# Performance work log

Hardware: AMD Instinct MI355X
Metric: run time of the kernel (lower is better)

## Reference

```python
import jax, jax.numpy as jnp
import numpy as np

B, C3, H3, W3 = 8, 512, 24, 24
C5, H5, W5 = 256, 96, 96
GRIDS = (6, 3, 2, 1)
GROUPS = 2


def conv2d(x, w):
    # stride-1 'same' conv (matches torch autopad k//2 for odd k), NCHW/OIHW
    return jax.lax.conv_general_dilated(x, w, (1, 1), 'SAME',
                                        dimension_numbers=('NCHW', 'OIHW', 'NCHW'))


def conv_bn_silu(x, w):
    # ultralytics-style Conv = Conv2d(bias=False) + BatchNorm2d + SiLU.
    # BN in eval with default running stats (mean=0, var=1, gamma=1, beta=0) is identity.
    return jax.nn.silu(conv2d(x, w))


def psp(x):
    # adaptive_avg_pool2d to (g, g) for each grid; H,W divisible by all grids -> equal bins
    b, c, h, w = x.shape
    outs = []
    for g in GRIDS:
        outs.append(x.reshape(b, c, g, h // g, g, w // g).mean(axis=(3, 5)).reshape(b, c, g * g))
    return jnp.concatenate(outs, axis=2)  # [b, c, 36+9+4+1=50]


def resize_bilinear_ac(x, oh, ow):
    # F.interpolate(mode='bilinear', align_corners=True)
    n, c, h, w = x.shape
    ys = jnp.linspace(0.0, h - 1.0, oh)
    xs = jnp.linspace(0.0, w - 1.0, ow)
    y0 = jnp.clip(jnp.floor(ys).astype(jnp.int32), 0, h - 2)
    x0 = jnp.clip(jnp.floor(xs).astype(jnp.int32), 0, w - 2)
    wy = (ys - y0)[None, None, :, None]
    wx = (xs - x0)[None, None, None, :]
    xr = jnp.take(x, y0, axis=2) * (1 - wy) + jnp.take(x, y0 + 1, axis=2) * wy
    return jnp.take(xr, x0, axis=3) * (1 - wx) + jnp.take(xr, x0 + 1, axis=3) * wx


def grid_sample(img, grid):
    # F.grid_sample bilinear, align_corners=True, padding_mode='zeros'
    # img [N,C,H,W], grid [N,Ho,Wo,2] with (x,y) normalized coords
    n, c, h, w = img.shape
    gx = (grid[..., 0] + 1.0) * 0.5 * (w - 1)
    gy = (grid[..., 1] + 1.0) * 0.5 * (h - 1)
    x0 = jnp.floor(gx)
    y0 = jnp.floor(gy)
    wx1 = gx - x0
    wy1 = gy - y0
    flat = img.reshape(n, c, h * w)

    def gather(xi, yi, wgt):
        valid = (xi >= 0) & (xi <= w - 1) & (yi >= 0) & (yi <= h - 1)
        xc = jnp.clip(xi, 0, w - 1).astype(jnp.int32)
        yc = jnp.clip(yi, 0, h - 1).astype(jnp.int32)
        idx = (yc * w + xc).reshape(n, 1, -1)
        v = jnp.take_along_axis(flat, idx, axis=2).reshape(n, c, grid.shape[1], grid.shape[2])
        return v * (wgt * valid)[:, None]

    return (gather(x0, y0, (1 - wx1) * (1 - wy1)) + gather(x0 + 1, y0, wx1 * (1 - wy1))
            + gather(x0, y0 + 1, (1 - wx1) * wy1) + gather(x0 + 1, y0 + 1, wx1 * wy1))


def _w(key, shape):
    fan_in = int(np.prod(shape[1:]))
    return (jax.random.normal(key, shape, jnp.float32) / np.sqrt(fan_in)).astype(jnp.float32)


def setup_inputs() -> dict:
    key = jax.random.key(0)
    ks = jax.random.split(key, 17)
    return {
        'p3': jax.random.normal(ks[0], (B, C3, H3, W3), jnp.float32),
        'p5': jax.random.normal(ks[1], (B, C5, H5, W5), jnp.float32),
        # CFC_CRB
        'w_red': _w(ks[2], (C3, C3, 3, 3)),
        'wq': _w(ks[3], (32, C3, 1, 1)), 'bq': jnp.zeros((32,), jnp.float32),
        'wk': _w(ks[4], (32, C3)), 'bk': jnp.zeros((32,), jnp.float32),
        'wv': _w(ks[5], (C3, C3)), 'bv': jnp.zeros((C3,), jnp.float32),
        'la_w1': _w(ks[6], (C3 // 8, C3, 1, 1)),
        'la_w2': _w(ks[7], (C3, C3 // 8, 3, 3)),
        # SFC_G2
        'w32': _w(ks[8], (C5, C3, 3, 3)),
        'w8': _w(ks[9], (C5, C5, 3, 3)),
        'woff1': _w(ks[10], (64, 2 * C5, 1, 1)),
        'woff2': _w(ks[11], (GROUPS * 4 + 2, 64, 3, 3)),
    }


def reference(p3, p5, w_red, wq, bq, wk, bk, wv, bv, la_w1, la_w2, w32, w8, woff1, woff2):
    # ---------------- CFC_CRB ----------------
    x = conv_bn_silu(p3, w_red)                      # [b,512,h,w]
    b, c, h, w = x.shape
    q = conv2d(x, wq) + bq[None, :, None, None]       # [b,32,h,w]
    q = q.reshape(b, 32, h * w).transpose(0, 2, 1)    # [b,N,32]
    kfeat = psp(x)                                    # [b,512,50]
    k = jnp.einsum('oc,bcm->bom', wk, kfeat) + bk[None, :, None]   # [b,32,50]
    sim = jax.nn.softmax(jnp.einsum('bnc,bcm->bnm', q, k), axis=-1)  # [b,N,50]
    v = jnp.einsum('oc,bcm->bom', wv, kfeat) + bv[None, :, None]   # [b,512,50]
    context = jnp.einsum('bcm,bnm->bcn', v, sim).reshape(b, c, h, w)
    # LocalAttenModule: res1 * tanh(conv(context)) + res2
    mask = jnp.tanh(conv2d(conv_bn_silu(context, la_w1), la_w2))
    context = context * mask + context
    p3o = x + context                                 # [b,512,24,24]

    # ---------------- SFC_G2 ----------------
    sp = conv_bn_silu(p3o, w32)                       # [b,256,24,24]
    sp = resize_bilinear_ac(sp, H5, W5)               # [b,256,96,96]
    cp = conv_bn_silu(p5, w8)                         # [b,256,96,96]
    cr = conv2d(conv_bn_silu(jnp.concatenate([cp, sp], axis=1), woff1), woff2)  # [b,10,96,96]

    n = b
    spg = sp.reshape(n * GROUPS, -1, H5, W5)
    cpg = cp.reshape(n * GROUPS, -1, H5, W5)
    off_l = cr[:, 0:GROUPS * 2].reshape(n * GROUPS, 2, H5, W5)
    off_h = cr[:, GROUPS * 2:GROUPS * 4].reshape(n * GROUPS, 2, H5, W5)

    gx = jnp.linspace(-1.0, 1.0, W5)
    gy = jnp.linspace(-1.0, 1.0, H5)
    X, Y = jnp.meshgrid(gx, gy)                       # [H5,W5] each
    base = jnp.stack([X, Y], axis=-1)[None]           # [1,H5,W5,2] (x,y)
    norm = jnp.array([W5, H5], dtype=sp.dtype)
    grid_l = base + off_l.transpose(0, 2, 3, 1) / norm
    grid_h = base + off_h.transpose(0, 2, 3, 1) / norm

    cps = grid_sample(cpg, grid_l).reshape(n, -1, H5, W5)
    sps = grid_sample(spg, grid_h).reshape(n, -1, H5, W5)
    att = 1.0 + jnp.tanh(cr[:, GROUPS * 4:])          # [b,2,H,W]
    p5o = sps * att[:, 0:1] + cps * att[:, 1:2]
    return (p3o, p5o)
```

## Files before the change

### kernel.cpp

```cpp
#include <hip/hip_runtime.h>
#include <math.h>

#define DI __device__ __forceinline__

typedef __attribute__((ext_vector_type(8))) short bf16x8;
typedef __attribute__((ext_vector_type(4))) float f32x4;

DI float silu_f(float v) { return v / (1.f + __expf(-v)); }
DI float4 ld4(const float* p) { return *reinterpret_cast<const float4*>(p); }
DI void st4(float* p, const float4& v) { *reinterpret_cast<float4*>(p) = v; }
DI unsigned short f2bf(float f) {
    unsigned u = __float_as_uint(f);
    unsigned r = (u + 0x7FFFu + ((u >> 16) & 1u)) >> 16;
    return (unsigned short)r;
}
DI float bf2f(unsigned short u) { return __uint_as_float(((unsigned)u) << 16); }

__global__ void pack_w2_kernel(const float* __restrict__ w, unsigned short* __restrict__ pk,
                               int Ci, int Co, int COG) {
    int idx = blockIdx.x * 256 + threadIdx.x;
    int total = Ci * Co * 9;
    if (idx >= total) return;
    int cc = idx & 31;
    int t = idx >> 5;
    int col = t % COG; t /= COG;
    int dydx = t % 9;  t /= 9;
    int nCoG = Co / COG;
    int cog = t % nCoG;
    int ch = t / nCoG;
    int co = cog * COG + col;
    pk[idx] = f2bf(w[((size_t)co * Ci + (ch << 5) + cc) * 9 + dydx]);
}

__global__ void pack_w1_kernel(const float* __restrict__ w, unsigned short* __restrict__ pk) {
    int idx = blockIdx.x * 256 + threadIdx.x;
    if (idx >= 32768) return;
    int cc = idx & 31;
    int col = (idx >> 5) & 63;
    int ch = idx >> 11;
    pk[idx] = f2bf(w[(size_t)col * 512 + (ch << 5) + cc]);
}

__global__ void pack_in_kernel(const float* __restrict__ in, unsigned short* __restrict__ pk,
                               int Ci, int HW, int total) {
    int idx = blockIdx.x * 256 + threadIdx.x;
    if (idx >= total) return;
    const int nCh = Ci >> 5;
    int cg = idx & 3;
    int t = idx >> 2;
    int pix = t % HW; t /= HW;
    int ch = t % nCh;
    int b = t / nCh;
    const float* src = in + ((size_t)b * Ci + (ch << 5) + (cg << 3)) * HW + pix;
    unsigned p[4];
#pragma unroll
    for (int j = 0; j < 4; ++j) {
        float v0 = src[(size_t)(2 * j) * HW];
        float v1 = src[(size_t)(2 * j + 1) * HW];
        p[j] = (unsigned)f2bf(v0) | ((unsigned)f2bf(v1) << 16);
    }
    *(uint4*)&pk[(((size_t)b * nCh + ch) * HW + pix) * 32 + (cg << 3)] =
        make_uint4(p[0], p[1], p[2], p[3]);
}

template <int TH, int TW, int BF, int WCO, int FUSE, int OUTPK>
__global__ void __launch_bounds__(256)
conv3x3_mfma2(const unsigned short* __restrict__ pin, const unsigned short* __restrict__ wpk,
              float* __restrict__ out, unsigned short* __restrict__ outpk,
              int B, int Ci, int Co, int H, int W,
              const float* __restrict__ ctx, const float* __restrict__ xres) {
    static_assert(TH * TW == 4 * BF * 16, "tile px = 4 waves * BF frags * 16");
    constexpr int COG = WCO * 16;
    constexpr int TWH = TW + 2;
    constexpr int HP = (TH + 2) * TWH;
    __shared__ __align__(16) unsigned short lin[HP * 40];

    const int nTx = W / TW, nTy = H / TH, nCoG = Co / COG;
    const int nwg = gridDim.x;
    int wg = (blockIdx.x & 7) * (nwg >> 3) + (blockIdx.x >> 3);
    const int cog = wg % nCoG; wg /= nCoG;
    const int tx = wg % nTx;   wg /= nTx;
    const int ty = wg % nTy;
    const int b = wg / nTy;
    const int ox = tx * TW, oy = ty * TH, co0 = cog * COG;

    const int tid = threadIdx.x;
    const int wave = tid >> 6, lane = tid & 63;
    const int l15 = lane & 15, g = lane >> 4;
    const int wpx = wave * (BF * 16);

    int rr[BF], cc_[BF];
#pragma unroll
    for (int bf = 0; bf < BF; ++bf) {
        int px = wpx + bf * 16 + l15;
        rr[bf] = px / TW;
        cc_[bf] = px % TW;
    }

    f32x4 acc[WCO][BF];
#pragma unroll
    for (int af = 0; af < WCO; ++af)
#pragma unroll
        for (int bf = 0; bf < BF; ++bf) acc[af][bf] = {};

    const int nCh = Ci >> 5;
    const size_t HWs = (size_t)H * W;

    for (int ch = 0; ch < nCh; ++ch) {
#pragma unroll
        for (int it = 0; it < (HP * 4 + 255) / 256; ++it) {
            int e = tid + it * 256;
            if (e < HP * 4) {
                int cg = e & 3;
                int hp = e >> 2;
                int hy = hp / TWH, hx = hp % TWH;
                int gy = oy + hy - 1, gx = ox + hx - 1;
                uint4 v = make_uint4(0, 0, 0, 0);
                if ((unsigned)gy < (unsigned)H && (unsigned)gx < (unsigned)W)
                    v = *(const uint4*)&pin[(((size_t)b * nCh + ch) * H * W
                                            + (size_t)gy * W + gx) * 32 + (cg << 3)];
                *(uint4*)&lin[hp * 40 + (cg << 3)] = v;
            }
        }
        __syncthreads();

        const unsigned short* wbase =
            wpk + ((((size_t)ch * nCoG + cog) * 9) * COG + l15) * 32 + g * 8;
#pragma unroll
        for (int dy = 0; dy < 3; ++dy) {
#pragma unroll
            for (int dx = 0; dx < 3; ++dx) {
                const int dydx = dy * 3 + dx;
                bf16x8 a[WCO];
#pragma unroll
                for (int af = 0; af < WCO; ++af)
                    a[af] = *(const bf16x8*)(wbase + ((size_t)dydx * COG + af * 16) * 32);
                bf16x8 bb[BF];
#pragma unroll
                for (int bf = 0; bf < BF; ++bf)
                    bb[bf] = *(const bf16x8*)&lin[((rr[bf] + dy) * TWH + cc_[bf] + dx) * 40 + g * 8];
#pragma unroll
                for (int af = 0; af < WCO; ++af)
#pragma unroll
                    for (int bf = 0; bf < BF; ++bf)
                        acc[af][bf] = __builtin_amdgcn_mfma_f32_16x16x32_bf16(
                            a[af], bb[bf], acc[af][bf], 0, 0, 0);
            }
        }
        __syncthreads();
    }
    const int nChO = Co >> 5;
#pragma unroll
    for (int af = 0; af < WCO; ++af) {
#pragma unroll
        for (int bf = 0; bf < BF; ++bf) {
            int px = wpx + bf * 16 + l15;
            int y = oy + px / TW, x = ox + px % TW;
            size_t pixg = (size_t)y * W + x;
            int coB = co0 + af * 16 + (g << 2);
            float vv[4];
#pragma unroll
            for (int r4 = 0; r4 < 4; ++r4) {
                float v = acc[af][bf][r4];
                if (FUSE == 1) v = silu_f(v);
                else if (FUSE == 2) {
                    size_t base = ((size_t)b * Co + coB + r4) * HWs + pixg;
                    v = xres[base] + ctx[base] * (1.f + tanhf(v));
                }
                vv[r4] = v;
            }
            if (OUTPK != 1) {
#pragma unroll
                for (int r4 = 0; r4 < 4; ++r4)
                    out[((size_t)b * Co + coB + r4) * HWs + pixg] = vv[r4];
            }
            if (OUTPK >= 1) {
                ushort4 s;
                s.x = f2bf(vv[0]); s.y = f2bf(vv[1]); s.z = f2bf(vv[2]); s.w = f2bf(vv[3]);
                *(ushort4*)&outpk[(((size_t)b * nChO + (coB >> 5)) * HWs + pixg) * 32 + (coB & 31)] = s;
            }
        }
    }
}

__global__ void __launch_bounds__(256)
cat_mfma(const unsigned short* __restrict__ cp_pk, const unsigned short* __restrict__ sp_pk,
         const unsigned short* __restrict__ wpk, float* __restrict__ out) {
    __shared__ __align__(16) unsigned short lin1[128 * 36];
    const int nwg = gridDim.x;
    int wg = (blockIdx.x & 7) * (nwg >> 3) + (blockIdx.x >> 3);
    int mt = wg % 72;
    int b = wg / 72;
    int m0 = mt * 128;
    const int tid = threadIdx.x;
    const int wave = tid >> 6, lane = tid & 63;
    const int l15 = lane & 15, g = lane >> 4;
    const int wpx = wave * 32;

    f32x4 acc[4][2];
#pragma unroll
    for (int af = 0; af < 4; ++af)
#pragma unroll
        for (int bf = 0; bf < 2; ++bf) acc[af][bf] = {};

    for (int ch = 0; ch < 16; ++ch) {
        const unsigned short* src = (ch < 8)
            ? cp_pk + (((size_t)b * 8 + ch) * 9216 + m0) * 32
            : sp_pk + (((size_t)b * 8 + ch - 8) * 9216 + m0) * 32;
#pragma unroll
        for (int it = 0; it < 2; ++it) {
            int e = tid + it * 256;
            int px = e >> 2, cg = e & 3;
            *(uint4*)&lin1[px * 36 + (cg << 3)] = *(const uint4*)&src[px * 32 + (cg << 3)];
        }
        __syncthreads();
        const unsigned short* wb = wpk + ((size_t)ch * 64 + l15) * 32 + g * 8;
        bf16x8 a[4];
#pragma unroll
        for (int af = 0; af < 4; ++af)
            a[af] = *(const bf16x8*)(wb + (af * 16) * 32);
        bf16x8 bb[2];
#pragma unroll
        for (int bf = 0; bf < 2; ++bf)
            bb[bf] = *(const bf16x8*)&lin1[(wpx + bf * 16 + l15) * 36 + g * 8];
#pragma unroll
        for (int af = 0; af < 4; ++af)
#pragma unroll
            for (int bf = 0; bf < 2; ++bf)
                acc[af][bf] = __builtin_amdgcn_mfma_f32_16x16x32_bf16(
                    a[af], bb[bf], acc[af][bf], 0, 0, 0);
        __syncthreads();
    }
#pragma unroll
    for (int af = 0; af < 4; ++af) {
#pragma unroll
        for (int bf = 0; bf < 2; ++bf) {
            int m = m0 + wpx + bf * 16 + l15;
#pragma unroll
            for (int r4 = 0; r4 < 4; ++r4) {
                int o = af * 16 + (g << 2) + r4;
                out[((size_t)b * 64 + o) * 9216 + m] = silu_f(acc[af][bf][r4]);
            }
        }
    }
}

DI void gs_params(int x, int y, float ox, float oy, float4* w, int2* p) {
    const float S = 47.5f / 96.f;
    float px = x + ox * S;
    float py = y + oy * S;
    float fx0 = floorf(px), fy0 = floorf(py);
    float wx = px - fx0, wy = py - fy0;
    float vx0 = (fx0 >= 0.f && fx0 <= 95.f) ? 1.f : 0.f;
    float vx1 = (fx0 >= -1.f && fx0 <= 94.f) ? 1.f : 0.f;
    float vy0 = (fy0 >= 0.f && fy0 <= 95.f) ? 1.f : 0.f;
    float vy1 = (fy0 >= -1.f && fy0 <= 94.f) ? 1.f : 0.f;
    int x0 = (int)fminf(fmaxf(fx0, 0.f), 95.f);
    int x1 = (int)fminf(fmaxf(fx0 + 1.f, 0.f), 95.f);
    int y0 = (int)fminf(fmaxf(fy0, 0.f), 95.f);
    int y1 = (int)fminf(fmaxf(fy0 + 1.f, 0.f), 95.f);
    w->x = (1.f - wx) * (1.f - wy) * vx0 * vy0;
    w->y = wx * (1.f - wy) * vx1 * vy0;
    w->z = (1.f - wx) * wy * vx0 * vy1;
    w->w = wx * wy * vx1 * vy1;
    *p = make_int2(x0 | (x1 << 16), y0 | (y1 << 16));
}

template <int TH, int TW, int CO_BLK, int CO_T, int CIC, int FUSE>
__global__ void __launch_bounds__(576)
conv3x3_kernel(const float* __restrict__ in, const float* __restrict__ wgt,
               float* __restrict__ out, int B, int Ci, int Co, int H, int W,
               float4* __restrict__ wpar, int2* __restrict__ ipk,
               float2* __restrict__ attp) {
    constexpr int TWH = TW + 2;
    constexpr int TWP = TW + 3;
    constexpr int SPAT = TH * (TW / 4);
    __shared__ float lin[CIC][TH + 2][TWP];
    __shared__ float wls[CIC][9][CO_BLK];
    __shared__ float crs[10][TH * TW + 1];

    const int nTx = W / TW, nTy = H / TH;
    const int nCoG = (Co + CO_BLK - 1) / CO_BLK;
    int bid = blockIdx.x;
    const int cog = bid % nCoG; bid /= nCoG;
    const int tx = bid % nTx;   bid /= nTx;
    const int ty = bid % nTy;
    const int b = bid / nTy;
    const int ox = tx * TW, oy = ty * TH;
    const int co0 = cog * CO_BLK;

    const int tid = threadIdx.x;
    const int cot = tid / SPAT;
    const int sp = tid % SPAT;
    const int r = sp / (TW / 4);
    const int cg = sp % (TW / 4);

    float acc[4][4];
#pragma unroll
    for (int i = 0; i < 4; ++i)
#pragma unroll
        for (int j = 0; j < 4; ++j) acc[i][j] = 0.f;

    for (int ci0 = 0; ci0 < Ci; ci0 += CIC) {
        for (int e = tid; e < CIC * (TH + 2) * TWH; e += SPAT * CO_T) {
            int xx = e % TWH;
            int yy = (e / TWH) % (TH + 2);
            int cc = e / (TWH * (TH + 2));
            int gy = oy - 1 + yy, gx = ox - 1 + xx;
            float v = 0.f;
            if (gy >= 0 && gy < H && gx >= 0 && gx < W)
                v = in[(((size_t)b * Ci + ci0 + cc) * H + gy) * W + gx];
            lin[cc][yy][xx] = v;
        }
        for (int e = tid; e < CIC * 9 * CO_BLK; e += SPAT * CO_T) {
            int col = e % CO_BLK;
            int k = (e / CO_BLK) % 9;
            int cc = e / (CO_BLK * 9);
            int co = co0 + col;
            float v = 0.f;
            if (co < Co) v = wgt[((size_t)co * Ci + ci0 + cc) * 9 + k];
            wls[cc][k][col] = v;
        }
        __syncthreads();
#pragma unroll
        for (int cc = 0; cc < CIC; ++cc) {
            float v0[3][6];
#pragma unroll
            for (int ky = 0; ky < 3; ++ky)
#pragma unroll
                for (int u = 0; u < 6; ++u)
                    v0[ky][u] = lin[cc][r + ky][cg * 4 + u];
#pragma unroll
            for (int ky = 0; ky < 3; ++ky)
#pragma unroll
                for (int kx = 0; kx < 3; ++kx) {
                    const float4 w4 = ld4(&wls[cc][ky * 3 + kx][cot * 4]);
                    const float wv_[4] = {w4.x, w4.y, w4.z, w4.w};
#pragma unroll
                    for (int i = 0; i < 4; ++i)
#pragma unroll
                        for (int j = 0; j < 4; ++j)
                            acc[i][j] = fmaf(wv_[i], v0[ky][kx + j], acc[i][j]);
                }
        }
        __syncthreads();
    }
    if (FUSE == 3) {
#pragma unroll
        for (int i = 0; i < 4; ++i) {
            int co = co0 + cot * 4 + i;
            if (co >= 10) continue;
#pragma unroll
            for (int j = 0; j < 4; ++j)
                crs[co][r * TW + cg * 4 + j] = acc[i][j];
        }
        __syncthreads();
        for (int e = tid; e < TH * TW; e += SPAT * CO_T) {
            int xx = ox + (e % TW), yy = oy + (e / TW);
            int pixg = yy * 96 + xx;
            float4 w; int2 p;
#pragma unroll
            for (int g2 = 0; g2 < 2; ++g2) {
                gs_params(xx, yy, crs[2 * g2][e], crs[2 * g2 + 1][e], &w, &p);
                size_t el = ((size_t)g2 * 8 + b) * 9216 + pixg;
                wpar[el] = w; ipk[el] = p;
                gs_params(xx, yy, crs[4 + 2 * g2][e], crs[5 + 2 * g2][e], &w, &p);
                size_t eh = ((size_t)(2 + g2) * 8 + b) * 9216 + pixg;
                wpar[eh] = w; ipk[eh] = p;
            }
            float2 at;
            at.x = 1.f + tanhf(crs[8][e]);
            at.y = 1.f + tanhf(crs[9][e]);
            attp[(size_t)b * 9216 + pixg] = at;
        }
    } else {
        const int y = oy + r;
        const int xb = ox + cg * 4;
#pragma unroll
        for (int i = 0; i < 4; ++i) {
            int co = co0 + cot * 4 + i;
            if (co >= Co) continue;
            size_t base = (((size_t)b * Co + co) * H + y) * W + xb;
            float4 res;
            res.x = acc[i][0]; res.y = acc[i][1]; res.z = acc[i][2]; res.w = acc[i][3];
            st4(&out[base], res);
        }
    }
}

template <int ACT, int PK>
__global__ void __launch_bounds__(256)
gemm_om(const float* __restrict__ W, const float* __restrict__ bias,
        const float* __restrict__ in, float* __restrict__ out,
        unsigned short* __restrict__ pko,
        int B, int C, int O, int M, int nOt, int nMt) {
    __shared__ float xs[32][66];
    __shared__ float wls[64][33];
    int bid = blockIdx.x;
    int mt = bid % nMt; bid /= nMt;
    int ot = bid % nOt;
    int b  = bid / nOt;
    int o0 = ot * 64, m0 = mt * 64;
    int tid = threadIdx.x;
    int m_t = tid & 15, o_g = tid >> 4;
    float acc[4][4];
#pragma unroll
    for (int i = 0; i < 4; ++i)
#pragma unroll
        for (int j = 0; j < 4; ++j) acc[i][j] = 0.f;

    for (int c0 = 0; c0 < C; c0 += 32) {
#pragma unroll
        for (int it = 0; it < 8; ++it) {
            int e = tid + it * 256;
            int mm = e & 63, cc = e >> 6;
            float v = 0.f;
            if (m0 + mm < M) v = in[((size_t)b * C + c0 + cc) * M + m0 + mm];
            xs[cc][mm] = v;
        }
#pragma unroll
        for (int it = 0; it < 8; ++it) {
            int e = tid + it * 256;
            int cc = e & 31, ol = e >> 5;
            float v = 0.f;
            if (o0 + ol < O) v = W[(size_t)(o0 + ol) * C + c0 + cc];
            wls[ol][cc] = v;
        }
        __syncthreads();
#pragma unroll
        for (int cc = 0; cc < 32; ++cc) {
            float xv[4], wv[4];
#pragma unroll
            for (int j = 0; j < 4; ++j) xv[j] = xs[cc][j * 16 + m_t];
#pragma unroll
            for (int i = 0; i < 4; ++i) wv[i] = wls[o_g * 4 + i][cc];
#pragma unroll
            for (int i = 0; i < 4; ++i)
#pragma unroll
                for (int j = 0; j < 4; ++j)
                    acc[i][j] = fmaf(wv[i], xv[j], acc[i][j]);
        }
        __syncthreads();
    }
#pragma unroll
    for (int i = 0; i < 4; ++i) {
        int o = o0 + o_g * 4 + i;
        if (o >= O) continue;
        float bv = bias ? bias[o] : 0.f;
#pragma unroll
        for (int j = 0; j < 4; ++j) {
            int m = m0 + j * 16 + m_t;
            if (m >= M) continue;
            float v = acc[i][j] + bv;
            if (ACT == 1) v = silu_f(v);
            if (PK)
                pko[(((size_t)b * (O >> 5) + (o >> 5)) * M + m) * 32 + (o & 31)] = f2bf(v);
            else
                out[((size_t)b * O + o) * M + m] = v;
        }
    }
}

__global__ void psp_kernel(const float* __restrict__ x, float* __restrict__ kf) {
    __shared__ float pl[576];
    int bc = blockIdx.x;
    const float* xp = x + (size_t)bc * 576;
    for (int e = threadIdx.x; e < 576; e += 64) pl[e] = xp[e];
    __syncthreads();
    int m = threadIdx.x;
    if (m < 50) {
        int g, i0;
        if (m < 36)      { g = 6; i0 = m; }
        else if (m < 45) { g = 3; i0 = m - 36; }
        else if (m < 49) { g = 2; i0 = m - 45; }
        else             { g = 1; i0 = 0; }
        int bs = 24 / g;
        int by = i0 / g, bx = i0 % g;
        float s = 0.f;
        for (int yy = 0; yy < bs; ++yy)
            for (int xx = 0; xx < bs; ++xx)
                s += pl[(by * bs + yy) * 24 + bx * bs + xx];
        kf[(size_t)bc * 50 + m] = s / (float)(bs * bs);
    }
}

__global__ void __launch_bounds__(256)
sim_kernel(const float* __restrict__ q, const float* __restrict__ k,
           float* __restrict__ simg) {
    __shared__ float qs[32][65];
    __shared__ float ks[32][52];
    __shared__ float sm[64][52];
    int b = blockIdx.x / 9, n0 = (blockIdx.x % 9) * 64;
    int tid = threadIdx.x;
    for (int e = tid; e < 32 * 64; e += 256) {
        int c = e >> 6, n = e & 63;
        qs[c][n] = q[((size_t)b * 32 + c) * 576 + n0 + n];
    }
    for (int e = tid; e < 32 * 50; e += 256) {
        int c = e / 50, m = e % 50;
        ks[c][m] = k[((size_t)b * 32 + c) * 50 + m];
    }
    __syncthreads();
    for (int e = tid; e < 64 * 50; e += 256) {
        int n = e / 50, m = e % 50;
        float s = 0.f;
#pragma unroll
        for (int c = 0; c < 32; ++c) s = fmaf(qs[c][n], ks[c][m], s);
        sm[n][m] = s;
    }
    __syncthreads();
    if (tid < 64) {
        float mx = -1e30f;
        for (int m = 0; m < 50; ++m) mx = fmaxf(mx, sm[tid][m]);
        float sum = 0.f;
        for (int m = 0; m < 50; ++m) {
            float e2 = __expf(sm[tid][m] - mx);
            sm[tid][m] = e2;
            sum += e2;
        }
        float inv = 1.f / sum;
        for (int m = 0; m < 50; ++m) sm[tid][m] *= inv;
    }
    __syncthreads();
    for (int e = tid; e < 64 * 50; e += 256) {
        int n = e / 50, m = e % 50;
        simg[((size_t)b * 576 + n0 + n) * 50 + m] = sm[n][m];
    }
}

__global__ void __launch_bounds__(256)
ctx_kernel(const float* __restrict__ v, const float* __restrict__ simg,
           float* __restrict__ ctx) {
    __shared__ float vs[128][54];
    __shared__ float ss[64][54];
    int blk = blockIdx.x;
    int ct = blk & 3; blk >>= 2;
    int nt = blk % 9;
    int b = blk / 9;
    int c0 = ct * 128, n0 = nt * 64;
    int tid = threadIdx.x;
    for (int e = tid; e < 128 * 50; e += 256) {
        int c = e / 50, m = e % 50;
        vs[c][m] = v[((size_t)b * 512 + c0 + c) * 50 + m];
    }
    for (int e = tid; e < 64 * 50; e += 256) {
        int n = e / 50, m = e % 50;
        ss[n][m] = simg[((size_t)b * 576 + n0 + n) * 50 + m];
    }
    __syncthreads();
    int n_t = tid & 15;
    int c_t = tid >> 4;
    float acc[8][4];
#pragma unroll
    for (int i = 0; i < 8; ++i)
#pragma unroll
        for (int j = 0; j < 4; ++j) acc[i][j] = 0.f;
    for (int m = 0; m < 50; ++m) {
        float sv[4];
#pragma unroll
        for (int j = 0; j < 4; ++j) sv[j] = ss[j * 16 + n_t][m];
#pragma unroll
        for (int i = 0; i < 8; ++i) {
            float vv = vs[c_t * 8 + i][m];
#pragma unroll
            for (int j = 0; j < 4; ++j) acc[i][j] = fmaf(vv, sv[j], acc[i][j]);
        }
    }
#pragma unroll
    for (int i = 0; i < 8; ++i)
#pragma unroll
        for (int j = 0; j < 4; ++j)
            ctx[((size_t)b * 512 + c0 + c_t * 8 + i) * 576 + n0 + j * 16 + n_t] = acc[i][j];
}

__global__ void upsample2_kernel(const float* __restrict__ in, unsigned short* __restrict__ outpk) {
    int idx = blockIdx.x * 256 + threadIdx.x;
    if (idx >= 8 * 8 * 4 * 9216) return;
    int cg = idx & 3;
    int t = idx >> 2;
    int pix = t % 9216; t /= 9216;
    int ch = t & 7;
    int b = t >> 3;
    int x = pix % 96, y = pix / 96;
    float fy = y * (23.f / 95.f);
    float fx = x * (23.f / 95.f);
    int y0 = (int)fy; if (y0 > 22) y0 = 22;
    int x0 = (int)fx; if (x0 > 22) x0 = 22;
    float wy = fy - y0, wx = fx - x0;
    const float* base = in + ((size_t)b * 256 + ch * 32 + cg * 8) * 576 + y0 * 24 + x0;
    unsigned short s[8];
#pragma unroll
    for (int j = 0; j < 8; ++j) {
        const float* ip = base + (size_t)j * 576;
        float a = ip[0], bb = ip[1], c = ip[24], d = ip[25];
        float l = a * (1.f - wy) + c * wy;
        float r = bb * (1.f - wy) + d * wy;
        s[j] = f2bf(l * (1.f - wx) + r * wx);
    }
    *(uint4*)&outpk[(((size_t)b * 8 + ch) * 9216 + pix) * 32 + cg * 8] =
        make_uint4((unsigned)s[0] | ((unsigned)s[1] << 16),
                   (unsigned)s[2] | ((unsigned)s[3] << 16),
                   (unsigned)s[4] | ((unsigned)s[5] << 16),
                   (unsigned)s[6] | ((unsigned)s[7] << 16));
}

__global__ void __launch_bounds__(256)
gsample3_kernel(const unsigned short* __restrict__ cp_pk, const unsigned short* __restrict__ sp_pk,
                const float4* __restrict__ wpar, const int2* __restrict__ ipk,
                const float2* __restrict__ attp, float* __restrict__ p5o) {
    int idx = blockIdx.x * 256 + threadIdx.x;
    if (idx >= 8 * 32 * 9216) return;
    int pix = idx % 9216;
    int cb = (idx / 9216) & 31;
    int b = idx / (9216 * 32);
    int c0 = cb * 8;
    int g = c0 >> 7, ch = c0 >> 5, coff = c0 & 31;
    size_t el = ((size_t)g * 8 + b) * 9216 + pix;
    size_t eh = ((size_t)(2 + g) * 8 + b) * 9216 + pix;
    float4 wl = wpar[el]; int2 pl = ipk[el];
    float4 wh = wpar[eh]; int2 ph = ipk[eh];
    float2 at = attp[(size_t)b * 9216 + pix];
    int l00 = (pl.y & 0xffff) * 96 + (pl.x & 0xffff);
    int l01 = (pl.y & 0xffff) * 96 + (pl.x >> 16);
    int l10 = (pl.y >> 16) * 96 + (pl.x & 0xffff);
    int l11 = (pl.y >> 16) * 96 + (pl.x >> 16);
    int h00 = (ph.y & 0xffff) * 96 + (ph.x & 0xffff);
    int h01 = (ph.y & 0xffff) * 96 + (ph.x >> 16);
    int h10 = (ph.y >> 16) * 96 + (ph.x & 0xffff);
    int h11 = (ph.y >> 16) * 96 + (ph.x >> 16);
    const unsigned short* cb0 = cp_pk + (((size_t)b * 8 + ch) * 9216) * 32 + coff;
    const unsigned short* sb0 = sp_pk + (((size_t)b * 8 + ch) * 9216) * 32 + coff;
    ushort4 tc0 = *(const ushort4*)&cb0[(size_t)l00 * 32];
    ushort4 tc0b = *(const ushort4*)&cb0[(size_t)l00 * 32 + 4];
    ushort4 tc1 = *(const ushort4*)&cb0[(size_t)l01 * 32];
    ushort4 tc1b = *(const ushort4*)&cb0[(size_t)l01 * 32 + 4];
    ushort4 tc2 = *(const ushort4*)&cb0[(size_t)l10 * 32];
    ushort4 tc2b = *(const ushort4*)&cb0[(size_t)l10 * 32 + 4];
    ushort4 tc3 = *(const ushort4*)&cb0[(size_t)l11 * 32];
    ushort4 tc3b = *(const ushort4*)&cb0[(size_t)l11 * 32 + 4];
    ushort4 ts0 = *(const ushort4*)&sb0[(size_t)h00 * 32];
    ushort4 ts0b = *(const ushort4*)&sb0[(size_t)h00 * 32 + 4];
    ushort4 ts1 = *(const ushort4*)&sb0[(size_t)h01 * 32];
    ushort4 ts1b = *(const ushort4*)&sb0[(size_t)h01 * 32 + 4];
    ushort4 ts2 = *(const ushort4*)&sb0[(size_t)h10 * 32];
    ushort4 ts2b = *(const ushort4*)&sb0[(size_t)h10 * 32 + 4];
    ushort4 ts3 = *(const ushort4*)&sb0[(size_t)h11 * 32];
    ushort4 ts3b = *(const ushort4*)&sb0[(size_t)h11 * 32 + 4];
    const unsigned short* c0a = (const unsigned short*)&tc0;
    const unsigned short* c0bp = (const unsigned short*)&tc0b;
    const unsigned short* c1a = (const unsigned short*)&tc1;
    const unsigned short* c1bp = (const unsigned short*)&tc1b;
    const unsigned short* c2a = (const unsigned short*)&tc2;
    const unsigned short* c2bp = (const unsigned short*)&tc2b;
    const unsigned short* c3a = (const unsigned short*)&tc3;
    const unsigned short* c3bp = (const unsigned short*)&tc3b;
    const unsigned short* s0a = (const unsigned short*)&ts0;
    const unsigned short* s0bp = (const unsigned short*)&ts0b;
    const unsigned short* s1a = (const unsigned short*)&ts1;
    const unsigned short* s1bp = (const unsigned short*)&ts1b;
    const unsigned short* s2a = (const unsigned short*)&ts2;
    const unsigned short* s2bp = (const unsigned short*)&ts2b;
    const unsigned short* s3a = (const unsigned short*)&ts3;
    const unsigned short* s3bp = (const unsigned short*)&ts3b;
    float* op = p5o + ((size_t)b * 256 + c0) * 9216 + pix;
#pragma unroll
    for (int i = 0; i < 8; ++i) {
        unsigned short v0 = (i < 4) ? c0a[i] : c0bp[i - 4];
        unsigned short v1 = (i < 4) ? c1a[i] : c1bp[i - 4];
        unsigned short v2 = (i < 4) ? c2a[i] : c2bp[i - 4];
        unsigned short v3 = (i < 4) ? c3a[i] : c3bp[i - 4];
        float cps = wl.x * bf2f(v0) + wl.y * bf2f(v1) + wl.z * bf2f(v2) + wl.w * bf2f(v3);
        unsigned short u0 = (i < 4) ? s0a[i] : s0bp[i - 4];
        unsigned short u1 = (i < 4) ? s1a[i] : s1bp[i - 4];
        unsigned short u2 = (i < 4) ? s2a[i] : s2bp[i - 4];
        unsigned short u3 = (i < 4) ? s3a[i] : s3bp[i - 4];
        float sps = wh.x * bf2f(u0) + wh.y * bf2f(u1) + wh.z * bf2f(u2) + wh.w * bf2f(u3);
        op[(size_t)i * 9216] = sps * at.x + cps * at.y;
    }
}

extern "C" void kernel_launch(void* const* d_in, const int* in_sizes, int n_in,
                              void* d_out, int out_size, void* d_ws, size_t ws_size,
                              hipStream_t stream) {
    const float* p3    = (const float*)d_in[0];
    const float* p5    = (const float*)d_in[1];
    const float* w_red = (const float*)d_in[2];
    const float* wq    = (const float*)d_in[3];
    const float* bq    = (const float*)d_in[4];
    const float* wk    = (const float*)d_in[5];
    const float* bk    = (const float*)d_in[6];
    const float* wv    = (const float*)d_in[7];
    const float* bv    = (const float*)d_in[8];
    const float* la_w1 = (const float*)d_in[9];
    const float* la_w2 = (const float*)d_in[10];
    const float* w32   = (const float*)d_in[11];
    const float* w8    = (const float*)d_in[12];
    const float* woff1 = (const float*)d_in[13];
    const float* woff2 = (const float*)d_in[14];

    float* out = (float*)d_out;
    float* p3o = out;
    float* p5o = out + 2359296;

    float* ws = (float*)d_ws;
    float* x_   = ws + 0;
    float* ctx  = ws + 2359296;
    float* q    = ws + 4718592;
    float* kf   = ws + 4866048;
    float* km   = ws + 5070848;
    float* vm   = ws + 5083648;
    unsigned short* la1_pk = (unsigned short*)(ws + 5288448);
    float* sp24 = ws + 5435904;
    float4* wpar = (float4*)(ws + 6615552);
    int2*   ipk  = (int2*)(ws + 7795200);
    float2* attp = (float2*)(ws + 8385024);
    unsigned short* sp96_pk = (unsigned short*)(ws + 8601600);
    unsigned short* cp_pk   = (unsigned short*)(ws + 18038784);
    unsigned short* p5_pk   = (unsigned short*)(ws + 27475968);
    unsigned short* p3_pk   = (unsigned short*)(ws + 36913152);
    unsigned short* wred_pk = (unsigned short*)(ws + 38092800);
    unsigned short* w32_pk  = (unsigned short*)(ws + 39272448);
    unsigned short* w8_pk   = (unsigned short*)(ws + 39862272);
    unsigned short* wla2_pk = (unsigned short*)(ws + 40157184);
    unsigned short* woff1_pk= (unsigned short*)(ws + 40304640);
    float* simg = ws + 5288448 + 160000;
    simg = ws + 40321024;
    float* t64  = ws + 0;

    pack_w2_kernel<<<dim3(2359296 / 256), dim3(256), 0, stream>>>(w_red, wred_pk, 512, 512, 32);
    pack_w2_kernel<<<dim3(1179648 / 256), dim3(256), 0, stream>>>(w32, w32_pk, 512, 256, 16);
    pack_w2_kernel<<<dim3(589824 / 256), dim3(256), 0, stream>>>(w8, w8_pk, 256, 256, 64);
    pack_w2_kernel<<<dim3(294912 / 256), dim3(256), 0, stream>>>(la_w2, wla2_pk, 64, 512, 32);
    pack_w1_kernel<<<dim3(128), dim3(256), 0, stream>>>(woff1, woff1_pk);
    pack_in_kernel<<<dim3(2359296 / 256), dim3(256), 0, stream>>>(p5, p5_pk, 256, 9216, 2359296);
    pack_in_kernel<<<dim3(294912 / 256), dim3(256), 0, stream>>>(p3, p3_pk, 512, 576, 294912);

    conv3x3_mfma2<16, 16, 4, 4, 1, 1><<<dim3(1152), dim3(256), 0, stream>>>(
        p5_pk, w8_pk, nullptr, cp_pk, 8, 256, 256, 96, 96, nullptr, nullptr);
    conv3x3_mfma2<8, 24, 3, 2, 1, 0><<<dim3(384), dim3(256), 0, stream>>>(
        p3_pk, wred_pk, x_, nullptr, 8, 512, 512, 24, 24, nullptr, nullptr);
    gemm_om<0, 0><<<dim3(72), dim3(256), 0, stream>>>(
        wq, bq, x_, q, nullptr, 8, 512, 32, 576, 1, 9);
    psp_kernel<<<dim3(8 * 512), dim3(64), 0, stream>>>(x_, kf);
    gemm_om<0, 0><<<dim3(8), dim3(256), 0, stream>>>(
        wk, bk, kf, km, nullptr, 8, 512, 32, 50, 1, 1);
    gemm_om<0, 0><<<dim3(64), dim3(256), 0, stream>>>(
        wv, bv, kf, vm, nullptr, 8, 512, 512, 50, 8, 1);
    sim_kernel<<<dim3(72), dim3(256), 0, stream>>>(q, km, simg);
    ctx_kernel<<<dim3(288), dim3(256), 0, stream>>>(vm, simg, ctx);
    gemm_om<1, 1><<<dim3(72), dim3(256), 0, stream>>>(
        la_w1, nullptr, ctx, nullptr, la1_pk, 8, 512, 64, 576, 1, 9);
    conv3x3_mfma2<8, 24, 3, 2, 2, 2><<<dim3(384), dim3(256), 0, stream>>>(
        la1_pk, wla2_pk, p3o, p3_pk, 8, 64, 512, 24, 24, ctx, x_);
    conv3x3_mfma2<8, 24, 3, 1, 1, 0><<<dim3(384), dim3(256), 0, stream>>>(
        p3_pk, w32_pk, sp24, nullptr, 8, 512, 256, 24, 24, nullptr, nullptr);
    upsample2_kernel<<<dim3(9216), dim3(256), 0, stream>>>(sp24, sp96_pk);
    cat_mfma<<<dim3(576), dim3(256), 0, stream>>>(cp_pk, sp96_pk, woff1_pk, t64);
    conv3x3_kernel<8, 32, 12, 3, 4, 3><<<dim3(288), dim3(192), 0, stream>>>(
        t64, woff2, nullptr, 8, 64, 10, 96, 96, wpar, ipk, attp);
    gsample3_kernel<<<dim3(9216), dim3(256), 0, stream>>>(
        cp_pk, sp96_pk, wpar, ipk, attp, p5o);
}
```

Baseline: 893.2 us.

## Double-buffer conv3x3 LDS staging with direct global-to-LDS loads on padded inputs

Packed bf16 conv inputs are now stored with a one-pixel zero border, so the 3x3 conv tiles can be staged without bounds checks. Staging uses global_load_lds straight into two ping-pong LDS buffers with an XOR swizzle, which lets the load of the next channel chunk overlap the MFMA work on the current one and halves the barriers. The cost is extra memsets of the padded buffers on every call, a larger workspace layout, and doubled LDS use that may lower occupancy.

```diff
diff --git a/kernel.cpp b/kernel.cpp
--- a/kernel.cpp
+++ b/kernel.cpp
@@ -15,6 +15,12 @@
     return (unsigned short)r;
 }
 DI float bf2f(unsigned short u) { return __uint_as_float(((unsigned)u) << 16); }
+
+DI void gload_lds16(const unsigned short* g, unsigned short* l) {
+    __builtin_amdgcn_global_load_lds(
+        (const __attribute__((address_space(1))) void*)g,
+        (__attribute__((address_space(3))) void*)l, 16, 0, 0);
+}
 
 __global__ void pack_w2_kernel(const float* __restrict__ w, unsigned short* __restrict__ pk,
                                int Ci, int Co, int COG) {
@@ -41,16 +47,18 @@
     pk[idx] = f2bf(w[(size_t)col * 512 + (ch << 5) + cc]);
 }
 
-__global__ void pack_in_kernel(const float* __restrict__ in, unsigned short* __restrict__ pk,
-                               int Ci, int HW, int total) {
+__global__ void pack_in_pad_kernel(const float* __restrict__ in, unsigned short* __restrict__ pk,
+                                   int Ci, int H, int W, int total) {
     int idx = blockIdx.x * 256 + threadIdx.x;
     if (idx >= total) return;
     const int nCh = Ci >> 5;
+    const int HW = H * W;
     int cg = idx & 3;
     int t = idx >> 2;
     int pix = t % HW; t /= HW;
     int ch = t % nCh;
     int b = t / nCh;
+    int y = pix / W, x = pix % W;
     const float* src = in + ((size_t)b * Ci + (ch << 5) + (cg << 3)) * HW + pix;
     unsigned p[4];
 #pragma unroll
@@ -59,13 +67,13 @@
         float v1 = src[(size_t)(2 * j + 1) * HW];
         p[j] = (unsigned)f2bf(v0) | ((unsigned)f2bf(v1) << 16);
     }
-    *(uint4*)&pk[(((size_t)b * nCh + ch) * HW + pix) * 32 + (cg << 3)] =
-        make_uint4(p[0], p[1], p[2], p[3]);
-}
-
-template <int TH, int TW, int BF, int WCO, int FUSE, int OUTPK>
+    size_t dst = (((size_t)b * nCh + ch) * (H + 2) + (y + 1)) * (W + 2) + (x + 1);
+    *(uint4*)&pk[dst * 32 + (cg << 3)] = make_uint4(p[0], p[1], p[2], p[3]);
+}
+
+template <int TH, int TW, int BF, int WCO, int FUSE, int OUTPK, int OUTPAD>
 __global__ void __launch_bounds__(256)
-conv3x3_mfma2(const unsigned short* __restrict__ pin, const unsigned short* __restrict__ wpk,
+conv3x3_mfma3(const unsigned short* __restrict__ pin, const unsigned short* __restrict__ wpk,
               float* __restrict__ out, unsigned short* __restrict__ outpk,
               int B, int Ci, int Co, int H, int W,
               const float* __restrict__ ctx, const float* __restrict__ xres) {
@@ -73,9 +81,14 @@
     constexpr int COG = WCO * 16;
     constexpr int TWH = TW + 2;
     constexpr int HP = (TH + 2) * TWH;
-    __shared__ __align__(16) unsigned short lin[HP * 40];
+    constexpr int NG = HP * 4;
+    constexpr int NIT = (NG + 255) / 256;
+    static_assert(NG % 8 == 0, "granules divisible by 8");
+    __shared__ __align__(16) unsigned short linA[NG * 8];
+    __shared__ __align__(16) unsigned short linB[NG * 8];
 
     const int nTx = W / TW, nTy = H / TH, nCoG = Co / COG;
+    const int Wp = W + 2, Hp = H + 2;
     const int nwg = gridDim.x;
     int wg = (blockIdx.x & 7) * (nwg >> 3) + (blockIdx.x >> 3);
     const int cog = wg % nCoG; wg /= nCoG;
@@ -85,9 +98,9 @@
     const int ox = tx * TW, oy = ty * TH, co0 = cog * COG;
 
     const int tid = threadIdx.x;
-    const int wave = tid >> 6, lane = tid & 63;
+    const int lane = tid & 63;
     const int l15 = lane & 15, g = lane >> 4;
-    const int wpx = wave * (BF * 16);
+    const int wpx = (tid >> 6) * (BF * 16);
 
     int rr[BF], cc_[BF];
 #pragma unroll
@@ -106,50 +119,72 @@
     const int nCh = Ci >> 5;
     const size_t HWs = (size_t)H * W;
 
-    for (int ch = 0; ch < nCh; ++ch) {
-#pragma unroll
-        for (int it = 0; it < (HP * 4 + 255) / 256; ++it) {
-            int e = tid + it * 256;
-            if (e < HP * 4) {
-                int cg = e & 3;
-                int hp = e >> 2;
-                int hy = hp / TWH, hx = hp % TWH;
-                int gy = oy + hy - 1, gx = ox + hx - 1;
-                uint4 v = make_uint4(0, 0, 0, 0);
-                if ((unsigned)gy < (unsigned)H && (unsigned)gx < (unsigned)W)
-                    v = *(const uint4*)&pin[(((size_t)b * nCh + ch) * H * W
-                                            + (size_t)gy * W + gx) * 32 + (cg << 3)];
-                *(uint4*)&lin[hp * 40 + (cg << 3)] = v;
-            }
-        }
+#define STAGE(DST, CH)                                                         \
+    {                                                                          \
+        const unsigned short* srcb =                                           \
+            pin + ((size_t)b * nCh + (CH)) * (size_t)Hp * Wp * 32;             \
+        _Pragma("unroll")                                                      \
+        for (int it = 0; it < NIT; ++it) {                                     \
+            int s = it * 256 + tid;                                            \
+            if (s < NG) {                                                      \
+                int e = s ^ ((s >> 3) & 7);                                    \
+                int hp = e >> 2, cgp = e & 3;                                  \
+                int hy = hp / TWH, hx = hp - hy * TWH;                         \
+                gload_lds16(srcb + ((size_t)(oy + hy) * Wp + (ox + hx)) * 32   \
+                                 + (cgp << 3),                                 \
+                            &(DST)[(s & ~63) << 3]);                           \
+            }                                                                  \
+        }                                                                      \
+    }
+
+#define COMPUTE(SRC, CH)                                                       \
+    {                                                                          \
+        const unsigned short* wbase =                                          \
+            wpk + ((((size_t)(CH) * nCoG + cog) * 9) * COG + l15) * 32 + (g << 3); \
+        _Pragma("unroll")                                                      \
+        for (int dy = 0; dy < 3; ++dy) {                                       \
+            _Pragma("unroll")                                                  \
+            for (int dx = 0; dx < 3; ++dx) {                                   \
+                const int dydx = dy * 3 + dx;                                  \
+                bf16x8 a[WCO];                                                 \
+                _Pragma("unroll")                                              \
+                for (int af = 0; af < WCO; ++af)                               \
+                    a[af] = *(const bf16x8*)(wbase + ((size_t)dydx * COG + af * 16) * 32); \
+                bf16x8 bb[BF];                                                 \
+                _Pragma("unroll")                                              \
+                for (int bf = 0; bf < BF; ++bf) {                              \
+                    int pxh = (rr[bf] + dy) * TWH + cc_[bf] + dx;              \
+                    int eg = (pxh << 2) | g;                                   \
+                    int slot = eg ^ ((eg >> 3) & 7);                           \
+                    bb[bf] = *(const bf16x8*)&(SRC)[slot << 3];                \
+                }                                                              \
+                _Pragma("unroll")                                              \
+                for (int af = 0; af < WCO; ++af)                               \
+                    _Pragma("unroll")                                          \
+                    for (int bf = 0; bf < BF; ++bf)                            \
+                        acc[af][bf] = __builtin_amdgcn_mfma_f32_16x16x32_bf16( \
+                            a[af], bb[bf], acc[af][bf], 0, 0, 0);              \
+            }                                                                  \
+        }                                                                      \
+    }
+
+    STAGE(linA, 0);
+    __syncthreads();
+    for (int chp = 0; chp < nCh; chp += 2) {
+        if (chp + 1 < nCh) STAGE(linB, chp + 1);
+        COMPUTE(linA, chp);
         __syncthreads();
-
-        const unsigned short* wbase =
-            wpk + ((((size_t)ch * nCoG + cog) * 9) * COG + l15) * 32 + g * 8;
-#pragma unroll
-        for (int dy = 0; dy < 3; ++dy) {
-#pragma unroll
-            for (int dx = 0; dx < 3; ++dx) {
-                const int dydx = dy * 3 + dx;
-                bf16x8 a[WCO];
-#pragma unroll
-                for (int af = 0; af < WCO; ++af)
-                    a[af] = *(const bf16x8*)(wbase + ((size_t)dydx * COG + af * 16) * 32);
-                bf16x8 bb[BF];
-#pragma unroll
-                for (int bf = 0; bf < BF; ++bf)
-                    bb[bf] = *(const bf16x8*)&lin[((rr[bf] + dy) * TWH + cc_[bf] + dx) * 40 + g * 8];
-#pragma unroll
-                for (int af = 0; af < WCO; ++af)
-#pragma unroll
-                    for (int bf = 0; bf < BF; ++bf)
-                        acc[af][bf] = __builtin_amdgcn_mfma_f32_16x16x32_bf16(
-                            a[af], bb[bf], acc[af][bf], 0, 0, 0);
-            }
-        }
-        __syncthreads();
-    }
+        if (chp + 1 < nCh) {
+            if (chp + 2 < nCh) STAGE(linA, chp + 2);
+            COMPUTE(linB, chp + 1);
+            __syncthreads();
+        }
+    }
+#undef STAGE
+#undef COMPUTE
+
     const int nChO = Co >> 5;
+    const size_t opitch = OUTPAD ? (size_t)(H + 2) * (W + 2) : HWs;
 #pragma unroll
     for (int af = 0; af < WCO; ++af) {
 #pragma unroll
@@ -177,7 +212,9 @@
             if (OUTPK >= 1) {
                 ushort4 s;
                 s.x = f2bf(vv[0]); s.y = f2bf(vv[1]); s.z = f2bf(vv[2]); s.w = f2bf(vv[3]);
-                *(ushort4*)&outpk[(((size_t)b * nChO + (coB >> 5)) * HWs + pixg) * 32 + (coB & 31)] = s;
+                size_t opix = OUTPAD ? ((size_t)(y + 1) * (W + 2) + (x + 1)) : pixg;
+                *(ushort4*)&outpk[(((size_t)b * nChO + (coB >> 5)) * opitch + opix) * 32
+                                  + (coB & 31)] = s;
             }
         }
     }
@@ -453,10 +490,13 @@
             if (m >= M) continue;
             float v = acc[i][j] + bv;
             if (ACT == 1) v = silu_f(v);
-            if (PK)
-                pko[(((size_t)b * (O >> 5) + (o >> 5)) * M + m) * 32 + (o & 31)] = f2bf(v);
-            else
+            if (PK) {
+                int yy = m / 24, xx = m % 24;
+                pko[(((size_t)b * (O >> 5) + (o >> 5)) * 676
+                     + (size_t)(yy + 1) * 26 + (xx + 1)) * 32 + (o & 31)] = f2bf(v);
+            } else {
                 out[((size_t)b * O + o) * M + m] = v;
+            }
         }
     }
 }
@@ -710,34 +750,37 @@
     float* km   = ws + 5070848;
     float* vm   = ws + 5083648;
     unsigned short* la1_pk = (unsigned short*)(ws + 5288448);
-    float* sp24 = ws + 5435904;
-    float4* wpar = (float4*)(ws + 6615552);
-    int2*   ipk  = (int2*)(ws + 7795200);
-    float2* attp = (float2*)(ws + 8385024);
-    unsigned short* sp96_pk = (unsigned short*)(ws + 8601600);
-    unsigned short* cp_pk   = (unsigned short*)(ws + 18038784);
-    unsigned short* p5_pk   = (unsigned short*)(ws + 27475968);
-    unsigned short* p3_pk   = (unsigned short*)(ws + 36913152);
-    unsigned short* wred_pk = (unsigned short*)(ws + 38092800);
-    unsigned short* w32_pk  = (unsigned short*)(ws + 39272448);
-    unsigned short* w8_pk   = (unsigned short*)(ws + 39862272);
-    unsigned short* wla2_pk = (unsigned short*)(ws + 40157184);
-    unsigned short* woff1_pk= (unsigned short*)(ws + 40304640);
-    float* simg = ws + 5288448 + 160000;
-    simg = ws + 40321024;
+    float* sp24 = ws + 5461504;
+    float4* wpar = (float4*)(ws + 6641152);
+    int2*   ipk  = (int2*)(ws + 7820800);
+    float2* attp = (float2*)(ws + 8410624);
+    float* simg = ws + 8558080;
+    unsigned short* sp96_pk = (unsigned short*)(ws + 8788480);
+    unsigned short* cp_pk   = (unsigned short*)(ws + 18225664);
+    unsigned short* p5_pk   = (unsigned short*)(ws + 27662848);
+    unsigned short* p3_pk   = (unsigned short*)(ws + 37497344);
+    unsigned short* wred_pk = (unsigned short*)(ws + 38881792);
+    unsigned short* w32_pk  = (unsigned short*)(ws + 40061440);
+    unsigned short* w8_pk   = (unsigned short*)(ws + 40651264);
+    unsigned short* wla2_pk = (unsigned short*)(ws + 40946176);
+    unsigned short* woff1_pk= (unsigned short*)(ws + 41093632);
     float* t64  = ws + 0;
+
+    hipMemsetAsync(p5_pk, 0, (size_t)8 * 8 * 98 * 98 * 32 * 2, stream);
+    hipMemsetAsync(p3_pk, 0, (size_t)8 * 16 * 676 * 32 * 2, stream);
+    hipMemsetAsync(la1_pk, 0, (size_t)8 * 2 * 676 * 32 * 2, stream);
 
     pack_w2_kernel<<<dim3(2359296 / 256), dim3(256), 0, stream>>>(w_red, wred_pk, 512, 512, 32);
     pack_w2_kernel<<<dim3(1179648 / 256), dim3(256), 0, stream>>>(w32, w32_pk, 512, 256, 16);
     pack_w2_kernel<<<dim3(589824 / 256), dim3(256), 0, stream>>>(w8, w8_pk, 256, 256, 64);
     pack_w2_kernel<<<dim3(294912 / 256), dim3(256), 0, stream>>>(la_w2, wla2_pk, 64, 512, 32);
     pack_w1_kernel<<<dim3(128), dim3(256), 0, stream>>>(woff1, woff1_pk);
-    pack_in_kernel<<<dim3(2359296 / 256), dim3(256), 0, stream>>>(p5, p5_pk, 256, 9216, 2359296);
-    pack_in_kernel<<<dim3(294912 / 256), dim3(256), 0, stream>>>(p3, p3_pk, 512, 576, 294912);
-
-    conv3x3_mfma2<16, 16, 4, 4, 1, 1><<<dim3(1152), dim3(256), 0, stream>>>(
+    pack_in_pad_kernel<<<dim3(9216), dim3(256), 0, stream>>>(p5, p5_pk, 256, 96, 96, 2359296);
+    pack_in_pad_kernel<<<dim3(1152), dim3(256), 0, stream>>>(p3, p3_pk, 512, 24, 24, 294912);
+
+    conv3x3_mfma3<16, 16, 4, 4, 1, 1, 0><<<dim3(1152), dim3(256), 0, stream>>>(
         p5_pk, w8_pk, nullptr, cp_pk, 8, 256, 256, 96, 96, nullptr, nullptr);
-    conv3x3_mfma2<8, 24, 3, 2, 1, 0><<<dim3(384), dim3(256), 0, stream>>>(
+    conv3x3_mfma3<8, 24, 3, 2, 1, 0, 0><<<dim3(384), dim3(256), 0, stream>>>(
         p3_pk, wred_pk, x_, nullptr, 8, 512, 512, 24, 24, nullptr, nullptr);
     gemm_om<0, 0><<<dim3(72), dim3(256), 0, stream>>>(
         wq, bq, x_, q, nullptr, 8, 512, 32, 576, 1, 9);
@@ -750,9 +793,9 @@
     ctx_kernel<<<dim3(288), dim3(256), 0, stream>>>(vm, simg, ctx);
     gemm_om<1, 1><<<dim3(72), dim3(256), 0, stream>>>(
         la_w1, nullptr, ctx, nullptr, la1_pk, 8, 512, 64, 576, 1, 9);
-    conv3x3_mfma2<8, 24, 3, 2, 2, 2><<<dim3(384), dim3(256), 0, stream>>>(
+    conv3x3_mfma3<8, 24, 3, 2, 2, 2, 1><<<dim3(384), dim3(256), 0, stream>>>(
         la1_pk, wla2_pk, p3o, p3_pk, 8, 64, 512, 24, 24, ctx, x_);
-    conv3x3_mfma2<8, 24, 3, 1, 1, 0><<<dim3(384), dim3(256), 0, stream>>>(
+    conv3x3_mfma3<8, 24, 3, 1, 1, 0, 0><<<dim3(384), dim3(256), 0, stream>>>(
         p3_pk, w32_pk, sp24, nullptr, 8, 512, 256, 24, 24, nullptr, nullptr);
     upsample2_kernel<<<dim3(9216), dim3(256), 0, stream>>>(sp24, sp96_pk);
     cat_mfma<<<dim3(576), dim3(256), 0, stream>>>(cp_pk, sp96_pk, woff1_pk, t64);
```

Result: no change. 904.1 us (+1.2%).
